# Kernel tuning notes

Measured on AMD Instinct MI355X. Metric: run time of the kernel, lower is better.

Reference implementation:

```python
import jax, jax.numpy as jnp
import numpy as np

NUM_CLASSES = 120
IN_C = 512
FILTERS = 512

def setup_inputs() -> dict:
    key = jax.random.key(0)
    k1, k2, k3, k4 = jax.random.split(key, 4)
    B, H, W = 32, 64, 64
    x = jax.random.normal(k1, (B, H, W, IN_C), dtype=jnp.float32)
    cls = jax.random.randint(k2, (B, 1), 0, NUM_CLASSES, dtype=jnp.int64)
    # kernel table: (num_classes, 1, 1, in_c, filters), glorot-like scale
    scale = (2.0 / (IN_C + FILTERS)) ** 0.5
    kernel = jax.random.normal(k3, (NUM_CLASSES, 1, 1, IN_C, FILTERS), dtype=jnp.float32) * scale
    bias = jnp.zeros((NUM_CLASSES, FILTERS), dtype=jnp.float32)
    return {"x": x, "cls": cls, "kernel": kernel, "bias": bias}

def reference(x, cls, kernel, bias):
    # x: [B,H,W,C] (channels_last), cls: [B,1] int ids
    c = jnp.squeeze(cls, axis=1)                      # [B]
    w = kernel[c, 0, 0]                               # [B, C, F] gathered per-sample kernel
    b = bias[c]                                       # [B, F]
    # per-sample 1x1 conv == batched matmul over pixels
    out = jnp.einsum('bhwc,bcf->bhwf', x, w)          # [B,H,W,F]
    out = out + b[:, None, None, :]
    return out
```

## Files before the change

### kernel.cpp

```cpp
#include <hip/hip_runtime.h>
#include <hip/hip_bf16.h>

typedef __bf16 bf16_t;
typedef __bf16 bf16x4 __attribute__((ext_vector_type(4)));
typedef __bf16 bf16x8 __attribute__((ext_vector_type(8)));
typedef float  f32x4  __attribute__((ext_vector_type(4)));

#define NB      32
#define NPIX    4096
#define CIN     512
#define FOUT    512
#define TM      128
#define TN      128
#define BK      32

__device__ __forceinline__ void async_copy16(const void* gsrc, void* ldsdst) {
    __builtin_amdgcn_global_load_lds(
        (const __attribute__((address_space(1))) unsigned int*)gsrc,
        (__attribute__((address_space(3))) unsigned int*)ldsdst,
        16, 0, 0);
}

__global__ __launch_bounds__(256) void gather_w_kernel(
    const float* __restrict__ kern, const int* __restrict__ cls,
    bf16_t* __restrict__ wsB)
{
    __shared__ float tile[32][33];
    const int n0 = blockIdx.x * 32;
    const int k0 = blockIdx.y * 32;
    const int b  = blockIdx.z;
    const int c  = cls[b];
    const int tx = threadIdx.x;
    const int ty = threadIdx.y;

    const float* src = kern + (long)c * CIN * FOUT;
#pragma unroll
    for (int i = 0; i < 4; i++) {
        int k = k0 + ty + i * 8;
        tile[ty + i * 8][tx] = src[(long)k * FOUT + n0 + tx];
    }
    __syncthreads();
    bf16_t* dst = wsB + (long)b * FOUT * CIN;
#pragma unroll
    for (int i = 0; i < 4; i++) {
        int n = n0 + ty + i * 8;
        dst[(long)n * CIN + k0 + tx] = (bf16_t)tile[tx][ty + i * 8];
    }
}

__global__ __launch_bounds__(256) void cond_conv_gemm(
    const float*  __restrict__ x,
    const bf16_t* __restrict__ wsB,
    const float*  __restrict__ bias,
    const int*    __restrict__ cls,
    float*        __restrict__ out)
{
    __shared__ float  AsF[TM * BK];
    __shared__ bf16_t BsH[TN * BK];

    const int hw  = blockIdx.x;
    const int bid = (hw & 7) * 512 + (hw >> 3);

    const int n_t = bid & 3;
    const int m_t = (bid >> 2) & 31;
    const int b   = bid >> 7;

    const long x_base = (long)b * NPIX * CIN + (long)m_t * TM * CIN;
    const long w_base = (long)b * FOUT * CIN;
    const int  n0     = n_t * TN;

    const int t    = threadIdx.x;
    const int wave = t >> 6;
    const int lane = t & 63;
    const int wm   = (wave >> 1) * 64;
    const int wn   = (wave & 1) * 64;
    const int l15  = lane & 15;
    const int quad = lane >> 4;

    f32x4 acc[4][4];
#pragma unroll
    for (int i = 0; i < 4; i++)
#pragma unroll
        for (int j = 0; j < 4; j++)
            acc[i][j] = (f32x4){0.f, 0.f, 0.f, 0.f};

    const int a_row_in_g = wave * 8 + (lane >> 3);
    const int a_kc       = ((lane & 7) ^ (lane >> 3)) << 2;
    const int b_row_in_g = wave * 16 + (lane >> 2);
    const int b_kc       = ((lane & 3) ^ ((lane >> 2) & 3)) << 3;

    for (int k0 = 0; k0 < CIN; k0 += BK) {
#pragma unroll
        for (int g = 0; g < 4; g++) {
            async_copy16(x + x_base + (long)(g * 32 + a_row_in_g) * CIN + k0 + a_kc,
                         (char*)AsF + g * 4096 + wave * 1024);
        }
#pragma unroll
        for (int g = 0; g < 2; g++) {
            async_copy16(wsB + w_base + (long)(n0 + g * 64 + b_row_in_g) * CIN + k0 + b_kc,
                         (char*)BsH + g * 4096 + wave * 1024);
        }
        __syncthreads();

        bf16x8 af[4], bfr[4];
#pragma unroll
        for (int i = 0; i < 4; i++) {
            int row = wm + i * 16 + l15;
            int r7  = row & 7;
            f32x4 a0 = *(const f32x4*)(&AsF[row * BK + ((( 2 * quad     ) ^ r7) << 2)]);
            f32x4 a1 = *(const f32x4*)(&AsF[row * BK + (((2 * quad + 1) ^ r7) << 2)]);
            bf16x8 h;
            h[0] = (bf16_t)a0[0]; h[1] = (bf16_t)a0[1];
            h[2] = (bf16_t)a0[2]; h[3] = (bf16_t)a0[3];
            h[4] = (bf16_t)a1[0]; h[5] = (bf16_t)a1[1];
            h[6] = (bf16_t)a1[2]; h[7] = (bf16_t)a1[3];
            af[i] = h;
        }
#pragma unroll
        for (int i = 0; i < 4; i++) {
            int row = wn + i * 16 + l15;
            bfr[i] = *(const bf16x8*)(&BsH[row * BK + ((quad ^ (row & 3)) << 3)]);
        }
#pragma unroll
        for (int mi = 0; mi < 4; mi++)
#pragma unroll
            for (int ni = 0; ni < 4; ni++)
                acc[mi][ni] = __builtin_amdgcn_mfma_f32_16x16x32_bf16(
                    af[mi], bfr[ni], acc[mi][ni], 0, 0, 0);
        __syncthreads();
    }

    const int c = cls[b];
    const long out_base = (long)b * NPIX * FOUT + (long)(m_t * TM) * FOUT + n0;
#pragma unroll
    for (int ni = 0; ni < 4; ni++) {
        float bv = bias[(long)c * FOUT + n0 + wn + ni * 16 + l15];
        int col = wn + ni * 16 + l15;
#pragma unroll
        for (int mi = 0; mi < 4; mi++) {
#pragma unroll
            for (int r = 0; r < 4; r++) {
                int row = wm + mi * 16 + quad * 4 + r;
                out[out_base + (long)row * FOUT + col] = acc[mi][ni][r] + bv;
            }
        }
    }
}

__global__ __launch_bounds__(256) void naive_kernel(
    const float* __restrict__ x, const float* __restrict__ kern,
    const float* __restrict__ bias, const int* __restrict__ cls,
    float* __restrict__ out)
{
    long i = (long)blockIdx.x * 256 + threadIdx.x;
    if (i >= (long)NB * NPIX * FOUT) return;
    int f = (int)(i % FOUT);
    long p = i / FOUT;
    int b = (int)(p / NPIX);
    int c = cls[b];
    const float* xr = x + p * CIN;
    const float* wc = kern + (long)c * CIN * FOUT + f;
    float acc = 0.f;
    for (int k = 0; k < CIN; k++) acc += xr[k] * wc[(long)k * FOUT];
    out[i] = acc + bias[(long)c * FOUT + f];
}

extern "C" void kernel_launch(void* const* d_in, const int* in_sizes, int n_in,
                              void* d_out, int out_size, void* d_ws, size_t ws_size,
                              hipStream_t stream)
{
    const float* x    = (const float*)d_in[0];
    const int*   cls  = (const int*)d_in[1];
    const float* kern = (const float*)d_in[2];
    const float* bias = (const float*)d_in[3];
    float*       out  = (float*)d_out;

    const size_t ws_need = (size_t)NB * FOUT * CIN * sizeof(bf16_t);
    if (ws_size >= ws_need) {
        bf16_t* wsB = (bf16_t*)d_ws;
        gather_w_kernel<<<dim3(FOUT / 32, CIN / 32, NB), dim3(32, 8), 0, stream>>>(
            kern, cls, wsB);
        cond_conv_gemm<<<NB * (NPIX / TM) * (FOUT / TN), 256, 0, stream>>>(
            x, wsB, bias, cls, out);
    } else {
        long n = (long)NB * NPIX * FOUT;
        naive_kernel<<<(int)((n + 255) / 256), 256, 0, stream>>>(x, kern, bias, cls, out);
    }
}
```

Measured before the change: 609.2 us.

## Load A directly to registers with prefetch, double-buffer B, vectorize output stores

The GEMM no longer stages the fp32 activation tile through LDS. Each lane reads its A fragment straight from global memory into registers, one k-step ahead, and converts it to bf16 after the MFMAs. The B tile is double-buffered in LDS so the next tile's async copy overlaps the current compute. The MFMA operands are swapped so each lane holds four consecutive output columns, which allows 16-byte vector stores and a vector bias load. In exchange there are uncoalesced-ish direct global reads of A (32B per lane per row) and higher register pressure from the prefetch buffers.

Result: slower. 684.4 us (+12.3%).

```diff
diff --git a/kernel.cpp b/kernel.cpp
--- a/kernel.cpp
+++ b/kernel.cpp
@@ -2,7 +2,6 @@
 #include <hip/hip_bf16.h>
 
 typedef __bf16 bf16_t;
-typedef __bf16 bf16x4 __attribute__((ext_vector_type(4)));
 typedef __bf16 bf16x8 __attribute__((ext_vector_type(8)));
 typedef float  f32x4  __attribute__((ext_vector_type(4)));
 
@@ -55,8 +54,7 @@
     const int*    __restrict__ cls,
     float*        __restrict__ out)
 {
-    __shared__ float  AsF[TM * BK];
-    __shared__ bf16_t BsH[TN * BK];
+    __shared__ bf16_t Bs[2][TN * BK];
 
     const int hw  = blockIdx.x;
     const int bid = (hw & 7) * 512 + (hw >> 3);
@@ -77,6 +75,14 @@
     const int l15  = lane & 15;
     const int quad = lane >> 4;
 
+    const int b_row_in_g = wave * 16 + (lane >> 2);
+    const int b_kc       = ((lane & 3) ^ ((lane >> 2) & 3)) << 3;
+
+    const float* a_ptr[4];
+#pragma unroll
+    for (int i = 0; i < 4; i++)
+        a_ptr[i] = x + x_base + (long)(wm + i * 16 + l15) * CIN + quad * 8;
+
     f32x4 acc[4][4];
 #pragma unroll
     for (int i = 0; i < 4; i++)
@@ -84,65 +90,84 @@
         for (int j = 0; j < 4; j++)
             acc[i][j] = (f32x4){0.f, 0.f, 0.f, 0.f};
 
-    const int a_row_in_g = wave * 8 + (lane >> 3);
-    const int a_kc       = ((lane & 7) ^ (lane >> 3)) << 2;
-    const int b_row_in_g = wave * 16 + (lane >> 2);
-    const int b_kc       = ((lane & 3) ^ ((lane >> 2) & 3)) << 3;
-
+#pragma unroll
+    for (int g = 0; g < 2; g++)
+        async_copy16(wsB + w_base + (long)(n0 + g * 64 + b_row_in_g) * CIN + b_kc,
+                     (char*)(&Bs[0][0]) + g * 4096 + wave * 1024);
+    bf16x8 af[4];
+#pragma unroll
+    for (int i = 0; i < 4; i++) {
+        f32x4 lo = *(const f32x4*)(a_ptr[i]);
+        f32x4 hi = *(const f32x4*)(a_ptr[i] + 4);
+        bf16x8 h;
+        h[0] = (bf16_t)lo[0]; h[1] = (bf16_t)lo[1];
+        h[2] = (bf16_t)lo[2]; h[3] = (bf16_t)lo[3];
+        h[4] = (bf16_t)hi[0]; h[5] = (bf16_t)hi[1];
+        h[6] = (bf16_t)hi[2]; h[7] = (bf16_t)hi[3];
+        af[i] = h;
+    }
+    __syncthreads();
+
+    int cur = 0;
     for (int k0 = 0; k0 < CIN; k0 += BK) {
-#pragma unroll
-        for (int g = 0; g < 4; g++) {
-            async_copy16(x + x_base + (long)(g * 32 + a_row_in_g) * CIN + k0 + a_kc,
-                         (char*)AsF + g * 4096 + wave * 1024);
-        }
-#pragma unroll
-        for (int g = 0; g < 2; g++) {
-            async_copy16(wsB + w_base + (long)(n0 + g * 64 + b_row_in_g) * CIN + k0 + b_kc,
-                         (char*)BsH + g * 4096 + wave * 1024);
-        }
-        __syncthreads();
-
-        bf16x8 af[4], bfr[4];
-#pragma unroll
-        for (int i = 0; i < 4; i++) {
-            int row = wm + i * 16 + l15;
-            int r7  = row & 7;
-            f32x4 a0 = *(const f32x4*)(&AsF[row * BK + ((( 2 * quad     ) ^ r7) << 2)]);
-            f32x4 a1 = *(const f32x4*)(&AsF[row * BK + (((2 * quad + 1) ^ r7) << 2)]);
-            bf16x8 h;
-            h[0] = (bf16_t)a0[0]; h[1] = (bf16_t)a0[1];
-            h[2] = (bf16_t)a0[2]; h[3] = (bf16_t)a0[3];
-            h[4] = (bf16_t)a1[0]; h[5] = (bf16_t)a1[1];
-            h[6] = (bf16_t)a1[2]; h[7] = (bf16_t)a1[3];
-            af[i] = h;
-        }
+        const int  kn       = k0 + BK;
+        const bool has_next = (kn < CIN);
+
+        if (has_next) {
+#pragma unroll
+            for (int g = 0; g < 2; g++)
+                async_copy16(wsB + w_base + (long)(n0 + g * 64 + b_row_in_g) * CIN + kn + b_kc,
+                             (char*)(&Bs[cur ^ 1][0]) + g * 4096 + wave * 1024);
+        }
+        f32x4 n_lo[4], n_hi[4];
+        if (has_next) {
+#pragma unroll
+            for (int i = 0; i < 4; i++) {
+                n_lo[i] = *(const f32x4*)(a_ptr[i] + kn);
+                n_hi[i] = *(const f32x4*)(a_ptr[i] + kn + 4);
+            }
+        }
+
+        bf16x8 bfr[4];
 #pragma unroll
         for (int i = 0; i < 4; i++) {
             int row = wn + i * 16 + l15;
-            bfr[i] = *(const bf16x8*)(&BsH[row * BK + ((quad ^ (row & 3)) << 3)]);
-        }
+            bfr[i] = *(const bf16x8*)(&Bs[cur][row * BK + ((quad ^ (row & 3)) << 3)]);
+        }
+
 #pragma unroll
         for (int mi = 0; mi < 4; mi++)
 #pragma unroll
             for (int ni = 0; ni < 4; ni++)
                 acc[mi][ni] = __builtin_amdgcn_mfma_f32_16x16x32_bf16(
-                    af[mi], bfr[ni], acc[mi][ni], 0, 0, 0);
+                    bfr[ni], af[mi], acc[mi][ni], 0, 0, 0);
+
+        if (has_next) {
+#pragma unroll
+            for (int i = 0; i < 4; i++) {
+                bf16x8 h;
+                h[0] = (bf16_t)n_lo[i][0]; h[1] = (bf16_t)n_lo[i][1];
+                h[2] = (bf16_t)n_lo[i][2]; h[3] = (bf16_t)n_lo[i][3];
+                h[4] = (bf16_t)n_hi[i][0]; h[5] = (bf16_t)n_hi[i][1];
+                h[6] = (bf16_t)n_hi[i][2]; h[7] = (bf16_t)n_hi[i][3];
+                af[i] = h;
+            }
+        }
+
         __syncthreads();
-    }
-
-    const int c = cls[b];
-    const long out_base = (long)b * NPIX * FOUT + (long)(m_t * TM) * FOUT + n0;
+        cur ^= 1;
+    }
+
+    const int  c        = cls[b];
+    const long out_row0 = (long)b * NPIX * FOUT + (long)(m_t * TM) * FOUT + n0;
 #pragma unroll
     for (int ni = 0; ni < 4; ni++) {
-        float bv = bias[(long)c * FOUT + n0 + wn + ni * 16 + l15];
-        int col = wn + ni * 16 + l15;
+        f32x4 bv = *(const f32x4*)(&bias[(long)c * FOUT + n0 + wn + ni * 16 + quad * 4]);
 #pragma unroll
         for (int mi = 0; mi < 4; mi++) {
-#pragma unroll
-            for (int r = 0; r < 4; r++) {
-                int row = wm + mi * 16 + quad * 4 + r;
-                out[out_base + (long)row * FOUT + col] = acc[mi][ni][r] + bv;
-            }
+            int m = wm + mi * 16 + l15;
+            f32x4 v = acc[mi][ni] + bv;
+            *(f32x4*)(&out[out_row0 + (long)m * FOUT + wn + ni * 16 + quad * 4]) = v;
         }
     }
 }
```

## Pre-convert activations to bf16 and use a bf16 GEMM with vectorized stores

Applied to the files above, without the earlier changes.

Adds a separate pass that converts x from fp32 to bf16 into workspace, then runs a GEMM that loads bf16 tiles for both operands. This halves the LDS footprint and global traffic per tile and removes the in-loop conversion. It also swaps the MFMA operands so each lane holds four consecutive output columns, which allows float4 stores of the output and float4 loads of the bias. The trade-off is an extra full read of x plus a write and re-read of a 128MB bf16 copy, and it needs a larger workspace, falling back to the mixed path otherwise.

Measured after the change: 652.9 us. 7.2% more time.

```diff
diff --git a/kernel.cpp b/kernel.cpp
--- a/kernel.cpp
+++ b/kernel.cpp
@@ -21,6 +21,25 @@
         16, 0, 0);
 }
 
+__global__ __launch_bounds__(256) void cvt_x_kernel(
+    const float* __restrict__ x, bf16_t* __restrict__ xb)
+{
+    const long n8 = (long)NB * NPIX * CIN / 8;
+    long i = (long)blockIdx.x * 256 + threadIdx.x;
+    const long stride = (long)gridDim.x * 256;
+    for (; i < n8; i += stride) {
+        const float* s = x + i * 8;
+        f32x4 lo = *(const f32x4*)(s);
+        f32x4 hi = *(const f32x4*)(s + 4);
+        bf16x8 h;
+        h[0] = (bf16_t)lo[0]; h[1] = (bf16_t)lo[1];
+        h[2] = (bf16_t)lo[2]; h[3] = (bf16_t)lo[3];
+        h[4] = (bf16_t)hi[0]; h[5] = (bf16_t)hi[1];
+        h[6] = (bf16_t)hi[2]; h[7] = (bf16_t)hi[3];
+        *(bf16x8*)(xb + i * 8) = h;
+    }
+}
+
 __global__ __launch_bounds__(256) void gather_w_kernel(
     const float* __restrict__ kern, const int* __restrict__ cls,
     bf16_t* __restrict__ wsB)
@@ -48,15 +67,15 @@
     }
 }
 
-__global__ __launch_bounds__(256) void cond_conv_gemm(
-    const float*  __restrict__ x,
+__global__ __launch_bounds__(256) void cond_conv_gemm_bf16(
+    const bf16_t* __restrict__ xb,
     const bf16_t* __restrict__ wsB,
     const float*  __restrict__ bias,
     const int*    __restrict__ cls,
     float*        __restrict__ out)
 {
-    __shared__ float  AsF[TM * BK];
-    __shared__ bf16_t BsH[TN * BK];
+    __shared__ bf16_t As[TM * BK];
+    __shared__ bf16_t Bs[TN * BK];
 
     const int hw  = blockIdx.x;
     const int bid = (hw & 7) * 512 + (hw >> 3);
@@ -65,7 +84,7 @@
     const int m_t = (bid >> 2) & 31;
     const int b   = bid >> 7;
 
-    const long x_base = (long)b * NPIX * CIN + (long)m_t * TM * CIN;
+    const long a_base = (long)b * NPIX * CIN + (long)m_t * TM * CIN;
     const long w_base = (long)b * FOUT * CIN;
     const int  n0     = n_t * TN;
 
@@ -77,6 +96,99 @@
     const int l15  = lane & 15;
     const int quad = lane >> 4;
 
+    const int st_row = t >> 2;
+    const int st_p   = t & 3;
+
+    f32x4 acc[4][4];
+#pragma unroll
+    for (int i = 0; i < 4; i++)
+#pragma unroll
+        for (int j = 0; j < 4; j++)
+            acc[i][j] = (f32x4){0.f, 0.f, 0.f, 0.f};
+
+    int a_off[2];
+#pragma unroll
+    for (int g = 0; g < 2; g++) {
+        int row = g * 64 + st_row;
+        int f   = (row + (row >> 2)) & 3;
+        a_off[g] = ((st_p - f) & 3) * 8;
+    }
+
+    for (int k0 = 0; k0 < CIN; k0 += BK) {
+#pragma unroll
+        for (int g = 0; g < 2; g++) {
+            int row = g * 64 + st_row;
+            async_copy16(xb + a_base + (long)row * CIN + k0 + a_off[g],
+                         (char*)As + g * 4096 + wave * 1024);
+            async_copy16(wsB + w_base + (long)(n0 + row) * CIN + k0 + a_off[g],
+                         (char*)Bs + g * 4096 + wave * 1024);
+        }
+        __syncthreads();
+
+        bf16x8 af[4], bfr[4];
+#pragma unroll
+        for (int i = 0; i < 4; i++) {
+            int row = wm + i * 16 + l15;
+            int p   = (quad + row + (row >> 2)) & 3;
+            af[i] = *(const bf16x8*)(&As[row * BK + p * 8]);
+        }
+#pragma unroll
+        for (int i = 0; i < 4; i++) {
+            int row = wn + i * 16 + l15;
+            int p   = (quad + row + (row >> 2)) & 3;
+            bfr[i] = *(const bf16x8*)(&Bs[row * BK + p * 8]);
+        }
+#pragma unroll
+        for (int mi = 0; mi < 4; mi++)
+#pragma unroll
+            for (int ni = 0; ni < 4; ni++)
+                acc[mi][ni] = __builtin_amdgcn_mfma_f32_16x16x32_bf16(
+                    bfr[ni], af[mi], acc[mi][ni], 0, 0, 0);
+        __syncthreads();
+    }
+
+    const int  c        = cls[b];
+    const long out_row0 = (long)b * NPIX * FOUT + (long)(m_t * TM) * FOUT + n0;
+#pragma unroll
+    for (int ni = 0; ni < 4; ni++) {
+        f32x4 bv = *(const f32x4*)(&bias[(long)c * FOUT + n0 + wn + ni * 16 + quad * 4]);
+#pragma unroll
+        for (int mi = 0; mi < 4; mi++) {
+            int m = wm + mi * 16 + l15;
+            f32x4 v = acc[mi][ni] + bv;
+            *(f32x4*)(&out[out_row0 + (long)m * FOUT + wn + ni * 16 + quad * 4]) = v;
+        }
+    }
+}
+
+__global__ __launch_bounds__(256) void cond_conv_gemm_mixed(
+    const float*  __restrict__ x,
+    const bf16_t* __restrict__ wsB,
+    const float*  __restrict__ bias,
+    const int*    __restrict__ cls,
+    float*        __restrict__ out)
+{
+    __shared__ float  AsF[TM * BK];
+    __shared__ bf16_t BsH[TN * BK];
+
+    const int hw  = blockIdx.x;
+    const int bid = (hw & 7) * 512 + (hw >> 3);
+    const int n_t = bid & 3;
+    const int m_t = (bid >> 2) & 31;
+    const int b   = bid >> 7;
+
+    const long x_base = (long)b * NPIX * CIN + (long)m_t * TM * CIN;
+    const long w_base = (long)b * FOUT * CIN;
+    const int  n0     = n_t * TN;
+
+    const int t    = threadIdx.x;
+    const int wave = t >> 6;
+    const int lane = t & 63;
+    const int wm   = (wave >> 1) * 64;
+    const int wn   = (wave & 1) * 64;
+    const int l15  = lane & 15;
+    const int quad = lane >> 4;
+
     f32x4 acc[4][4];
 #pragma unroll
     for (int i = 0; i < 4; i++)
@@ -91,15 +203,13 @@
 
     for (int k0 = 0; k0 < CIN; k0 += BK) {
 #pragma unroll
-        for (int g = 0; g < 4; g++) {
+        for (int g = 0; g < 4; g++)
             async_copy16(x + x_base + (long)(g * 32 + a_row_in_g) * CIN + k0 + a_kc,
                          (char*)AsF + g * 4096 + wave * 1024);
-        }
-#pragma unroll
-        for (int g = 0; g < 2; g++) {
+#pragma unroll
+        for (int g = 0; g < 2; g++)
             async_copy16(wsB + w_base + (long)(n0 + g * 64 + b_row_in_g) * CIN + k0 + b_kc,
                          (char*)BsH + g * 4096 + wave * 1024);
-        }
         __syncthreads();
 
         bf16x8 af[4], bfr[4];
@@ -107,7 +217,7 @@
         for (int i = 0; i < 4; i++) {
             int row = wm + i * 16 + l15;
             int r7  = row & 7;
-            f32x4 a0 = *(const f32x4*)(&AsF[row * BK + ((( 2 * quad     ) ^ r7) << 2)]);
+            f32x4 a0 = *(const f32x4*)(&AsF[row * BK + (((2 * quad)     ^ r7) << 2)]);
             f32x4 a1 = *(const f32x4*)(&AsF[row * BK + (((2 * quad + 1) ^ r7) << 2)]);
             bf16x8 h;
             h[0] = (bf16_t)a0[0]; h[1] = (bf16_t)a0[1];
@@ -126,23 +236,20 @@
 #pragma unroll
             for (int ni = 0; ni < 4; ni++)
                 acc[mi][ni] = __builtin_amdgcn_mfma_f32_16x16x32_bf16(
-                    af[mi], bfr[ni], acc[mi][ni], 0, 0, 0);
+                    bfr[ni], af[mi], acc[mi][ni], 0, 0, 0);
         __syncthreads();
     }
 
-    const int c = cls[b];
-    const long out_base = (long)b * NPIX * FOUT + (long)(m_t * TM) * FOUT + n0;
+    const int  c        = cls[b];
+    const long out_row0 = (long)b * NPIX * FOUT + (long)(m_t * TM) * FOUT + n0;
 #pragma unroll
     for (int ni = 0; ni < 4; ni++) {
-        float bv = bias[(long)c * FOUT + n0 + wn + ni * 16 + l15];
-        int col = wn + ni * 16 + l15;
+        f32x4 bv = *(const f32x4*)(&bias[(long)c * FOUT + n0 + wn + ni * 16 + quad * 4]);
 #pragma unroll
         for (int mi = 0; mi < 4; mi++) {
-#pragma unroll
-            for (int r = 0; r < 4; r++) {
-                int row = wm + mi * 16 + quad * 4 + r;
-                out[out_base + (long)row * FOUT + col] = acc[mi][ni][r] + bv;
-            }
+            int m = wm + mi * 16 + l15;
+            f32x4 v = acc[mi][ni] + bv;
+            *(f32x4*)(&out[out_row0 + (long)m * FOUT + wn + ni * 16 + quad * 4]) = v;
         }
     }
 }
@@ -175,12 +282,22 @@
     const float* bias = (const float*)d_in[3];
     float*       out  = (float*)d_out;
 
-    const size_t ws_need = (size_t)NB * FOUT * CIN * sizeof(bf16_t);
-    if (ws_size >= ws_need) {
+    const size_t xb_bytes = (size_t)NB * NPIX * CIN * sizeof(bf16_t);
+    const size_t w_bytes  = (size_t)NB * FOUT * CIN * sizeof(bf16_t);
+
+    if (ws_size >= xb_bytes + w_bytes) {
+        bf16_t* xbf = (bf16_t*)d_ws;
+        bf16_t* wsB = xbf + (size_t)NB * NPIX * CIN;
+        cvt_x_kernel<<<2048, 256, 0, stream>>>(x, xbf);
+        gather_w_kernel<<<dim3(FOUT / 32, CIN / 32, NB), dim3(32, 8), 0, stream>>>(
+            kern, cls, wsB);
+        cond_conv_gemm_bf16<<<NB * (NPIX / TM) * (FOUT / TN), 256, 0, stream>>>(
+            xbf, wsB, bias, cls, out);
+    } else if (ws_size >= w_bytes) {
         bf16_t* wsB = (bf16_t*)d_ws;
         gather_w_kernel<<<dim3(FOUT / 32, CIN / 32, NB), dim3(32, 8), 0, stream>>>(
             kern, cls, wsB);
-        cond_conv_gemm<<<NB * (NPIX / TM) * (FOUT / TN), 256, 0, stream>>>(
+        cond_conv_gemm_mixed<<<NB * (NPIX / TM) * (FOUT / TN), 256, 0, stream>>>(
             x, wsB, bias, cls, out);
     } else {
         long n = (long)NB * NPIX * FOUT;
```
